# Optimization experiments

Hardware: AMD Instinct MI355X
Metric: run time of the kernel (lower is better)

Reference implementation:

```python
import jax, jax.numpy as jnp
import numpy as np

# Instant-NGP / tcnn hash grid encoding constants (from init_kwargs)
L = 16           # n_levels
F = 2            # n_features_per_level
T = 2 ** 15      # hashmap size per level
DIM = 3
BASE = 16.0      # base_resolution
FINEST = 512.0   # finest_resolution
RANGE = 1.0
B = (FINEST / BASE) ** (1.0 / (L - 1))  # per_level_scale
N_POINTS = 500000
# tcnn spatial hash primes (first dim uses 1)
PRIMES = jnp.array([1, 2654435761, 805459861], dtype=jnp.uint32)


def setup_inputs() -> dict:
    key = jax.random.key(0)
    k1, k2 = jax.random.split(key)
    x = jax.random.uniform(k1, (N_POINTS, DIM), dtype=jnp.float32)  # points in [0,1)
    table = jax.random.normal(k2, (L, T, F), dtype=jnp.float32) * 1e-4  # tcnn-style tiny init
    return {"x": x, "table": table}


def reference(x, table):
    # wrapper: map from [-range, range] to [0, 1]
    xn = (x + RANGE) / (2.0 * RANGE)                       # [N, 3]
    n = xn.shape[0]
    # per-level grid scale (tcnn: scale = base * b^l - 1)
    scales = BASE * (B ** jnp.arange(L, dtype=jnp.float32)) - 1.0  # [L]
    pos = xn[:, None, :] * scales[None, :, None] + 0.5     # [N, L, 3]
    pos_floor = jnp.floor(pos)
    frac = pos - pos_floor                                  # [N, L, 3]
    grid = pos_floor.astype(jnp.uint32)                    # [N, L, 3]
    # 8 cube corners as binary offsets
    corners = jnp.array([[(c >> d) & 1 for d in range(DIM)] for c in range(2 ** DIM)],
                        dtype=jnp.uint32)                   # [8, 3]
    coords = grid[:, :, None, :] + corners[None, None, :, :]  # [N, L, 8, 3] uint32
    h = coords * PRIMES                                     # uint32 wraps (modular mult)
    idx = (h[..., 0] ^ h[..., 1] ^ h[..., 2]) & jnp.uint32(T - 1)  # [N, L, 8]
    # gather per-level features: [N, L, 8, F]
    feats = table[jnp.arange(L)[None, :, None], idx]
    # trilinear interpolation weights
    cf = corners.astype(jnp.float32)                        # [8, 3]
    w = jnp.prod(jnp.where(cf[None, None, :, :] == 1.0,
                           frac[:, :, None, :],
                           1.0 - frac[:, :, None, :]), axis=-1)  # [N, L, 8]
    out = jnp.einsum('nlc,nlcf->nlf', w, feats)             # [N, L, F]
    return out.reshape(n, L * F)
```

## Files before the change

### kernel.cpp

```cpp
#include <hip/hip_runtime.h>
#include <hip/hip_fp16.h>
#include <stdint.h>


constexpr int      kL  = 16;
constexpr int      kT  = 32768;
constexpr uint32_t kM  = kT - 1;
constexpr uint32_t kP1 = 2654435761u;
constexpr uint32_t kP2 = 805459861u;
constexpr int      kNC = 16;
constexpr int      kBT = 1024;

typedef float f32x2 __attribute__((ext_vector_type(2)));

__device__ __constant__ float c_scales[kL] = {
    15.0f,
    19.158736798317972f,
    24.398416831491190f,
    31.0f,
    39.317473596635944f,
    49.796833662982380f,
    63.0f,
    79.634947193271890f,
    100.59366732596477f,
    127.0f,
    160.26989438654378f,
    202.18733465192953f,
    255.0f,
    321.53978877308750f,
    405.37466930385903f,
    511.0f
};

__device__ __forceinline__ void unpack_h2(uint32_t u, float& lo, float& hi) {
    __half2 h = *reinterpret_cast<__half2*>(&u);
    lo = __low2float(h);
    hi = __high2float(h);
}

__global__ __launch_bounds__(kBT, 4) void hashgrid_fwd(
    const float*  __restrict__ x,
    const float2* __restrict__ table,
    f32x2*        __restrict__ out,
    int n_points, int chunk_sz)
{
    __shared__ uint32_t ltab[kT];

    int bid = blockIdx.x;
    int l   = bid >> 4;
    int c   = bid & 15;

    const float2* tsrc = table + (size_t)l * kT;
    for (int e = threadIdx.x; e < kT; e += kBT) {
        float2 f = tsrc[e];
        uint32_t p = ((uint32_t)__half_as_ushort(__float2half_rn(f.y)) << 16)
                   |  (uint32_t)__half_as_ushort(__float2half_rn(f.x));
        ltab[e] = p;
    }
    __syncthreads();

    float s = c_scales[l];
    int base = c * chunk_sz;
    int lim  = min(base + chunk_sz, n_points);

    for (int n = base + (int)threadIdx.x; n < lim; n += kBT) {
        float x0 = x[n * 3 + 0];
        float x1 = x[n * 3 + 1];
        float x2 = x[n * 3 + 2];

        float p0 = fmaf((x0 + 1.0f) * 0.5f, s, 0.5f);
        float p1 = fmaf((x1 + 1.0f) * 0.5f, s, 0.5f);
        float p2 = fmaf((x2 + 1.0f) * 0.5f, s, 0.5f);

        float fl0 = floorf(p0), fl1 = floorf(p1), fl2 = floorf(p2);
        float fr0 = p0 - fl0,   fr1 = p1 - fl1,   fr2 = p2 - fl2;

        uint32_t g0 = (uint32_t)(int)fl0;
        uint32_t g1 = (uint32_t)(int)fl1;
        uint32_t g2 = (uint32_t)(int)fl2;

        uint32_t hy0 = g1 * kP1;  uint32_t hy1 = hy0 + kP1;
        uint32_t hz0 = g2 * kP2;  uint32_t hz1 = hz0 + kP2;

        float wy0 = 1.0f - fr1, wz0 = 1.0f - fr2;
        float wx0 = 1.0f - fr0, wx1 = fr0;

        uint32_t hyz[4];
        float    wyz[4];
        hyz[0] = hy0 ^ hz0;  wyz[0] = wy0 * wz0;
        hyz[1] = hy1 ^ hz0;  wyz[1] = fr1 * wz0;
        hyz[2] = hy0 ^ hz1;  wyz[2] = wy0 * fr2;
        hyz[3] = hy1 ^ hz1;  wyz[3] = fr1 * fr2;

        float acc_x = 0.0f, acc_y = 0.0f;

        if (!(g0 & 1u)) {
#pragma unroll
            for (int j = 0; j < 4; ++j) {
                uint32_t i0 = (g0 ^ hyz[j]) & kM;
                uint32_t pb = i0 & ~1u;
                uint64_t two = *reinterpret_cast<const uint64_t*>(&ltab[pb]);
                uint32_t e0 = (uint32_t)two, e1 = (uint32_t)(two >> 32);
                bool sw = (i0 & 1u);
                uint32_t u0 = sw ? e1 : e0;
                uint32_t u1 = sw ? e0 : e1;
                float a0, b0, a1, b1;
                unpack_h2(u0, a0, b0);
                unpack_h2(u1, a1, b1);
                float fx = fmaf(wx0, a0, wx1 * a1);
                float fy = fmaf(wx0, b0, wx1 * b1);
                acc_x = fmaf(wyz[j], fx, acc_x);
                acc_y = fmaf(wyz[j], fy, acc_y);
            }
        } else {
            uint32_t g0p = g0 + 1u;
#pragma unroll
            for (int j = 0; j < 4; ++j) {
                uint32_t i0 = (g0  ^ hyz[j]) & kM;
                uint32_t i1 = (g0p ^ hyz[j]) & kM;
                uint32_t u0 = ltab[i0];
                uint32_t u1 = ltab[i1];
                float a0, b0, a1, b1;
                unpack_h2(u0, a0, b0);
                unpack_h2(u1, a1, b1);
                float fx = fmaf(wx0, a0, wx1 * a1);
                float fy = fmaf(wx0, b0, wx1 * b1);
                acc_x = fmaf(wyz[j], fx, acc_x);
                acc_y = fmaf(wyz[j], fy, acc_y);
            }
        }

        f32x2 r; r.x = acc_x; r.y = acc_y;
        out[(size_t)n * kL + l] = r;
    }
}

extern "C" void kernel_launch(void* const* d_in, const int* in_sizes, int n_in,
                              void* d_out, int out_size, void* d_ws, size_t ws_size,
                              hipStream_t stream) {
    const float*  x     = (const float*)d_in[0];
    const float2* table = (const float2*)d_in[1];
    f32x2*        out   = (f32x2*)d_out;

    int n_points = in_sizes[0] / 3;
    int chunk_sz = (n_points + kNC - 1) / kNC;
    int blocks   = kL * kNC;

    hashgrid_fwd<<<blocks, kBT, 0, stream>>>(x, table, out, n_points, chunk_sz);
}
```

Baseline: 50.42 us.

## Process two points per thread with batched LDS gathers, drop parity branch

Each thread now handles two points per loop iteration, computes all 16 hash indices and weights up front, then issues all 16 LDS reads together before interpolating. This exposes more independent LDS loads to hide their latency. It also removes the even/odd branch and its 64-bit paired read, so every corner is a plain 32-bit LDS load, which cuts divergence but issues more LDS instructions. Table staging now reads float4 and writes pairs of packed half2 values. More live registers under launch_bounds(1024,4) risks spilling.

```diff
diff --git a/kernel.cpp b/kernel.cpp
--- a/kernel.cpp
+++ b/kernel.cpp
@@ -32,12 +32,6 @@
     511.0f
 };
 
-__device__ __forceinline__ void unpack_h2(uint32_t u, float& lo, float& hi) {
-    __half2 h = *reinterpret_cast<__half2*>(&u);
-    lo = __low2float(h);
-    hi = __high2float(h);
-}
-
 __global__ __launch_bounds__(kBT, 4) void hashgrid_fwd(
     const float*  __restrict__ x,
     const float2* __restrict__ table,
@@ -50,12 +44,15 @@
     int l   = bid >> 4;
     int c   = bid & 15;
 
-    const float2* tsrc = table + (size_t)l * kT;
-    for (int e = threadIdx.x; e < kT; e += kBT) {
-        float2 f = tsrc[e];
-        uint32_t p = ((uint32_t)__half_as_ushort(__float2half_rn(f.y)) << 16)
-                   |  (uint32_t)__half_as_ushort(__float2half_rn(f.x));
-        ltab[e] = p;
+    const float4* tsrc4 = reinterpret_cast<const float4*>(table + (size_t)l * kT);
+    for (int e = threadIdx.x; e < kT / 2; e += kBT) {
+        float4 q = tsrc4[e];
+        uint2 pp;
+        pp.x = ((uint32_t)__half_as_ushort(__float2half_rn(q.y)) << 16)
+             |  (uint32_t)__half_as_ushort(__float2half_rn(q.x));
+        pp.y = ((uint32_t)__half_as_ushort(__float2half_rn(q.w)) << 16)
+             |  (uint32_t)__half_as_ushort(__float2half_rn(q.z));
+        *reinterpret_cast<uint2*>(&ltab[e * 2]) = pp;
     }
     __syncthreads();
 
@@ -63,75 +60,83 @@
     int base = c * chunk_sz;
     int lim  = min(base + chunk_sz, n_points);
 
-    for (int n = base + (int)threadIdx.x; n < lim; n += kBT) {
-        float x0 = x[n * 3 + 0];
-        float x1 = x[n * 3 + 1];
-        float x2 = x[n * 3 + 2];
+    for (int n0 = base + (int)threadIdx.x; n0 < lim; n0 += 2 * kBT) {
+        int nn[2];
+        nn[0] = n0;
+        int nB = n0 + kBT;
+        bool hasB = nB < lim;
+        nn[1] = hasB ? nB : n0;
 
-        float p0 = fmaf((x0 + 1.0f) * 0.5f, s, 0.5f);
-        float p1 = fmaf((x1 + 1.0f) * 0.5f, s, 0.5f);
-        float p2 = fmaf((x2 + 1.0f) * 0.5f, s, 0.5f);
+        uint32_t idx[2][8];
+        float    w[2][8];
 
-        float fl0 = floorf(p0), fl1 = floorf(p1), fl2 = floorf(p2);
-        float fr0 = p0 - fl0,   fr1 = p1 - fl1,   fr2 = p2 - fl2;
+#pragma unroll
+        for (int p = 0; p < 2; ++p) {
+            int n = nn[p];
+            float x0 = x[n * 3 + 0];
+            float x1 = x[n * 3 + 1];
+            float x2 = x[n * 3 + 2];
 
-        uint32_t g0 = (uint32_t)(int)fl0;
-        uint32_t g1 = (uint32_t)(int)fl1;
-        uint32_t g2 = (uint32_t)(int)fl2;
+            float p0 = fmaf((x0 + 1.0f) * 0.5f, s, 0.5f);
+            float p1 = fmaf((x1 + 1.0f) * 0.5f, s, 0.5f);
+            float p2 = fmaf((x2 + 1.0f) * 0.5f, s, 0.5f);
 
-        uint32_t hy0 = g1 * kP1;  uint32_t hy1 = hy0 + kP1;
-        uint32_t hz0 = g2 * kP2;  uint32_t hz1 = hz0 + kP2;
+            float fl0 = floorf(p0), fl1 = floorf(p1), fl2 = floorf(p2);
+            float fr0 = p0 - fl0,   fr1 = p1 - fl1,   fr2 = p2 - fl2;
 
-        float wy0 = 1.0f - fr1, wz0 = 1.0f - fr2;
-        float wx0 = 1.0f - fr0, wx1 = fr0;
+            uint32_t g0 = (uint32_t)(int)fl0;
+            uint32_t g1 = (uint32_t)(int)fl1;
+            uint32_t g2 = (uint32_t)(int)fl2;
 
-        uint32_t hyz[4];
-        float    wyz[4];
-        hyz[0] = hy0 ^ hz0;  wyz[0] = wy0 * wz0;
-        hyz[1] = hy1 ^ hz0;  wyz[1] = fr1 * wz0;
-        hyz[2] = hy0 ^ hz1;  wyz[2] = wy0 * fr2;
-        hyz[3] = hy1 ^ hz1;  wyz[3] = fr1 * fr2;
+            uint32_t hx0 = g0;        uint32_t hx1 = g0 + 1u;
+            uint32_t hy0 = g1 * kP1;  uint32_t hy1 = hy0 + kP1;
+            uint32_t hz0 = g2 * kP2;  uint32_t hz1 = hz0 + kP2;
 
-        float acc_x = 0.0f, acc_y = 0.0f;
+            float wy0 = 1.0f - fr1, wz0 = 1.0f - fr2;
+            float wx0 = 1.0f - fr0;
 
-        if (!(g0 & 1u)) {
+            float wyz[4];
+            wyz[0] = wy0 * wz0;
+            wyz[1] = fr1 * wz0;
+            wyz[2] = wy0 * fr2;
+            wyz[3] = fr1 * fr2;
+
+            uint32_t hyz[4];
+            hyz[0] = hy0 ^ hz0;
+            hyz[1] = hy1 ^ hz0;
+            hyz[2] = hy0 ^ hz1;
+            hyz[3] = hy1 ^ hz1;
+
 #pragma unroll
-            for (int j = 0; j < 4; ++j) {
-                uint32_t i0 = (g0 ^ hyz[j]) & kM;
-                uint32_t pb = i0 & ~1u;
-                uint64_t two = *reinterpret_cast<const uint64_t*>(&ltab[pb]);
-                uint32_t e0 = (uint32_t)two, e1 = (uint32_t)(two >> 32);
-                bool sw = (i0 & 1u);
-                uint32_t u0 = sw ? e1 : e0;
-                uint32_t u1 = sw ? e0 : e1;
-                float a0, b0, a1, b1;
-                unpack_h2(u0, a0, b0);
-                unpack_h2(u1, a1, b1);
-                float fx = fmaf(wx0, a0, wx1 * a1);
-                float fy = fmaf(wx0, b0, wx1 * b1);
-                acc_x = fmaf(wyz[j], fx, acc_x);
-                acc_y = fmaf(wyz[j], fy, acc_y);
-            }
-        } else {
-            uint32_t g0p = g0 + 1u;
-#pragma unroll
-            for (int j = 0; j < 4; ++j) {
-                uint32_t i0 = (g0  ^ hyz[j]) & kM;
-                uint32_t i1 = (g0p ^ hyz[j]) & kM;
-                uint32_t u0 = ltab[i0];
-                uint32_t u1 = ltab[i1];
-                float a0, b0, a1, b1;
-                unpack_h2(u0, a0, b0);
-                unpack_h2(u1, a1, b1);
-                float fx = fmaf(wx0, a0, wx1 * a1);
-                float fy = fmaf(wx0, b0, wx1 * b1);
-                acc_x = fmaf(wyz[j], fx, acc_x);
-                acc_y = fmaf(wyz[j], fy, acc_y);
+            for (int cc = 0; cc < 8; ++cc) {
+                uint32_t hx = (cc & 1) ? hx1 : hx0;
+                idx[p][cc] = (hx ^ hyz[cc >> 1]) & kM;
+                w[p][cc]   = ((cc & 1) ? fr0 : wx0) * wyz[cc >> 1];
             }
         }
 
-        f32x2 r; r.x = acc_x; r.y = acc_y;
-        out[(size_t)n * kL + l] = r;
+        uint32_t e[2][8];
+#pragma unroll
+        for (int p = 0; p < 2; ++p)
+#pragma unroll
+            for (int cc = 0; cc < 8; ++cc)
+                e[p][cc] = ltab[idx[p][cc]];
+
+        f32x2 r[2];
+#pragma unroll
+        for (int p = 0; p < 2; ++p) {
+            float acc_x = 0.0f, acc_y = 0.0f;
+#pragma unroll
+            for (int cc = 0; cc < 8; ++cc) {
+                __half2 h = *reinterpret_cast<__half2*>(&e[p][cc]);
+                acc_x = fmaf(w[p][cc], __low2float(h),  acc_x);
+                acc_y = fmaf(w[p][cc], __high2float(h), acc_y);
+            }
+            r[p].x = acc_x; r[p].y = acc_y;
+        }
+
+        out[(size_t)nn[0] * kL + l] = r[0];
+        if (hasB) out[(size_t)nn[1] * kL + l] = r[1];
     }
 }
 
```

New measurement: 49.31 us. 2.2% less time.
